# Performance work log

Measured on AMD Instinct MI355X. Metric: run time of the kernel, lower is better.

Reference implementation:

```python
import jax, jax.numpy as jnp
import numpy as np

B, S, D, H, E = 8, 2048, 1024, 4096, 8


def setup_inputs() -> dict:
    key = jax.random.key(0)
    k0, k1, k2, k3 = jax.random.split(key, 4)
    x = jax.random.normal(k0, (B, S, D), dtype=jnp.float32)
    # hash-router assignment: one expert per token, shape [B, S, 1] (top-k dim k=1)
    assign = jax.random.randint(k1, (B, S, 1), 0, E, dtype=jnp.int64)
    # per-expert Linear(dim, hidden): W_e [E, D, H], b_e [E, H]
    W_e = jax.random.normal(k2, (E, D, H), dtype=jnp.float32) * (1.0 / np.sqrt(D))
    b_e = jnp.zeros((E, H), dtype=jnp.float32)
    # shared output Linear(hidden, dim)
    W_out = jax.random.normal(k3, (H, D), dtype=jnp.float32) * (1.0 / np.sqrt(H))
    b_out = jnp.zeros((D,), dtype=jnp.float32)
    return {"x": x, "W_e": W_e, "b_e": b_e, "W_out": W_out, "b_out": b_out,
            "assign": assign}


def reference(x, W_e, b_e, W_out, b_out, assign):
    num_experts = W_e.shape[0]
    hidden = W_e.shape[2]
    # zero-init combine buffer, matching torch.zeros(batch, seq, hidden)
    expert_out = jnp.zeros(x.shape[:2] + (hidden,), dtype=x.dtype)
    for e in range(num_experts):  # fixed small expert loop
        y = jnp.einsum("bsd,dh->bsh", x, W_e[e]) + b_e[e]
        mask = (assign == e).any(-1)  # [B, S]
        expert_out = jnp.where(mask[..., None], y, expert_out)
    h = jax.nn.relu(expert_out)
    return jnp.einsum("bsh,hd->bsd", h, W_out) + b_out
```

## Files before the change

### kernel.cpp

```cpp
#include <hip/hip_runtime.h>
#include <hip/hip_bf16.h>
#include <stdint.h>

#define NB 8
#define NS 2048
#define ND 1024
#define NH 4096
#define NE 8
#define NTOK (NB*NS)

typedef __bf16 bf16;
typedef bf16 bf16x8 __attribute__((ext_vector_type(8)));
typedef float f32x4 __attribute__((ext_vector_type(4)));

static const size_t OFF_XB  = 128 * 1024;
static const size_t OFF_WTE = OFF_XB  + (size_t)NTOK * ND * 2;
static const size_t OFF_WTO = OFF_WTE + (size_t)NE * NH * ND * 2;
static const size_t OFF_HB  = OFF_WTO + (size_t)ND * NH * 2;
static const size_t WS_NEED = OFF_HB  + (size_t)NTOK * NH * 2;

#define GLDS16(src, dst) __builtin_amdgcn_global_load_lds( \
    (__attribute__((address_space(1))) void*)(void*)(src), \
    (__attribute__((address_space(3))) void*)(dst), 16, 0, 0)


__global__ void k_route(const int* __restrict__ assign, int* __restrict__ meta) {
    __shared__ int cnt[NE];
    __shared__ int offs_s[NE];
    int tid = threadIdx.x;
    if (tid < NE) cnt[tid] = 0;
    __syncthreads();
    for (int t = tid; t < NTOK; t += 1024) atomicAdd(&cnt[assign[t] & 7], 1);
    __syncthreads();
    if (tid == 0) {
        int o = 0;
        for (int e = 0; e < NE; e++) {
            meta[e] = cnt[e]; meta[16 + e] = o; offs_s[e] = o; o += cnt[e];
        }
    }
    __syncthreads();
    if (tid < NE) cnt[tid] = offs_s[tid];
    __syncthreads();
    int* perm = meta + 512;
    for (int t = tid; t < NTOK; t += 1024) {
        int e = assign[t] & 7;
        int p = atomicAdd(&cnt[e], 1);
        perm[p] = t;
    }
}

__global__ void k_gather_cvt(const float* __restrict__ x, const int* __restrict__ meta,
                             bf16* __restrict__ xbp) {
    long i = (long)blockIdx.x * blockDim.x + threadIdx.x;
    int row = (int)(i >> 7);
    int c8  = (int)(i & 127);
    const int* perm = meta + 512;
    int tok = perm[row];
    const float4* s = (const float4*)(x + (size_t)tok * ND + c8 * 8);
    float4 v0 = s[0], v1 = s[1];
    bf16x8 o;
    o[0] = (bf16)v0.x; o[1] = (bf16)v0.y; o[2] = (bf16)v0.z; o[3] = (bf16)v0.w;
    o[4] = (bf16)v1.x; o[5] = (bf16)v1.y; o[6] = (bf16)v1.z; o[7] = (bf16)v1.w;
    *(bf16x8*)(xbp + i * 8) = o;
}

__global__ void k_transpose(const float* __restrict__ in, bf16* __restrict__ out,
                            int R, int C) {
    __shared__ float tile[32][33];
    int b  = blockIdx.z;
    int c0 = blockIdx.x * 32, r0 = blockIdx.y * 32;
    const float* inb = in + (size_t)b * R * C;
    bf16* outb = out + (size_t)b * R * C;
    int tx = threadIdx.x, ty = threadIdx.y;
#pragma unroll
    for (int i = 0; i < 4; i++) {
        int r = r0 + ty + i * 8;
        tile[ty + i * 8][tx] = inb[(size_t)r * C + c0 + tx];
    }
    __syncthreads();
#pragma unroll
    for (int i = 0; i < 4; i++) {
        int c = c0 + ty + i * 8;
        outb[(size_t)c * R + r0 + tx] = (bf16)tile[tx][ty + i * 8];
    }
}


#define BAR { __builtin_amdgcn_s_barrier(); asm volatile("" ::: "memory"); }
#define VMC8 asm volatile("s_waitcnt vmcnt(8)" ::: "memory")
#define VMC0 asm volatile("s_waitcnt vmcnt(0)" ::: "memory")

#define LDA(msub) { \
  const char* Ab = sm + abuf + wr * 16384; \
  _Pragma("unroll") for (int m = 0; m < 4; m++) { \
    int row = ((msub) * 4 + m) * 16 + lr; \
    af[m][0] = *(const bf16x8*)(Ab + row * 128 + xk0); \
    af[m][1] = *(const bf16x8*)(Ab + row * 128 + xk1); \
  } }

#define LDB(nsub) { \
  const char* Bb = sm + bbuf + (wc >> 1) * 16384; \
  _Pragma("unroll") for (int n = 0; n < 2; n++) { \
    int row = (wc & 1) * 64 + ((nsub) * 2 + n) * 16 + lr; \
    bfr[(nsub)*2+n][0] = *(const bf16x8*)(Bb + row * 128 + xk0); \
    bfr[(nsub)*2+n][1] = *(const bf16x8*)(Bb + row * 128 + xk1); \
  } }

#define MFMA_Q(msub, nsub) { \
  __builtin_amdgcn_s_setprio(1); \
  _Pragma("unroll") for (int m = 0; m < 4; m++) \
  _Pragma("unroll") for (int n = 0; n < 2; n++) \
  _Pragma("unroll") for (int k = 0; k < 2; k++) \
    acc[(msub)*4+m][(nsub)*2+n] = __builtin_amdgcn_mfma_f32_16x16x32_bf16( \
        af[m][k], bfr[(nsub)*2+n][k], acc[(msub)*4+m][(nsub)*2+n], 0, 0, 0); \
  __builtin_amdgcn_s_setprio(0); }

#define DO_TILE(i, S0, S1, S2, S3, VW) { \
  const int abuf = ((i) % 3) * 32768; \
  const int bbuf = 98304 + ((i) & 1) * 32768; \
  LDA(0); LDB(0); S0; BAR; MFMA_Q(0,0); BAR; \
  LDB(1);         S1; BAR; MFMA_Q(0,1); BAR; \
  LDA(1);         S2; BAR; MFMA_Q(1,0); BAR; \
                  S3; VW; BAR; MFMA_Q(1,1); BAR; \
}

#define STAGE_A(t, h) { \
    char* d = sm + ((t) % 3) * 32768 + (h) * 16384 + wid * 1024; \
    GLDS16(srcA(t, h, 0), d); \
    GLDS16(srcA(t, h, 1), d + 8192); }
#define STAGE_B(t, h) { \
    char* d = sm + 98304 + ((t) & 1) * 32768 + (h) * 16384 + wid * 1024; \
    GLDS16(srcB(t, h, 0), d); \
    GLDS16(srcB(t, h, 1), d + 8192); }

__launch_bounds__(512, 2)
__global__ void k_gemm1(const bf16* __restrict__ xbp, const bf16* __restrict__ wte,
                        const float* __restrict__ b_e, bf16* __restrict__ hb,
                        const int* __restrict__ meta) {
    __shared__ __align__(16) char sm[163840];
    int f = blockIdx.x;
    int e = f & 7, q = f >> 3;
    int j = q % 9, bx = q / 9;
    int cnt = meta[e];
    int rs  = meta[16 + e] + j * 256;
    int rc  = cnt - j * 256; if (rc > 256) rc = 256;
    if (rc <= 0) return;
    int n0 = bx * 256;

    int tid = threadIdx.x;
    int lane = tid & 63, wid = tid >> 6;
    int wr = wid >> 2, wc = wid & 3;
    int lr = lane & 15, kg = lane >> 4;
    int xk0 = (kg ^ (lr & 7)) * 16;
    int xk1 = ((4 + kg) ^ (lr & 7)) * 16;

    int sr = tid >> 3, sl = tid & 7;
    int g = sl ^ (sr & 7);
    const bf16* pa[2][2];
#pragma unroll
    for (int h = 0; h < 2; h++)
#pragma unroll
      for (int rr = 0; rr < 2; rr++) {
        int arow = h * 128 + rr * 64 + sr;
        int p = rs + (arow < rc - 1 ? arow : rc - 1);
        pa[h][rr] = xbp + (size_t)p * ND + g * 8;
      }
    const bf16* pb0 = wte + ((size_t)e * NH + n0 + sr) * ND + g * 8;

#define srcA(t, h, rr) (pa[h][rr] + (size_t)(t) * 64)
#define srcB(t, h, rr) (pb0 + ((h) * 128 + (rr) * 64) * (size_t)ND + (size_t)(t) * 64)

    f32x4 acc[8][4] = {};
    bf16x8 af[4][2], bfr[4][2];
    const int NT = ND / 64;

    STAGE_A(0, 0); STAGE_A(0, 1); STAGE_B(0, 0); STAGE_B(0, 1);
    STAGE_A(1, 0); STAGE_A(1, 1); STAGE_B(1, 0); STAGE_B(1, 1);
    VMC8;
    BAR;

#pragma unroll 6
    for (int i = 0; i < NT - 2; i++)
        DO_TILE(i, STAGE_A(i + 2, 0), STAGE_A(i + 2, 1),
                   STAGE_B(i + 2, 0), STAGE_B(i + 2, 1), VMC8);
    DO_TILE(NT - 2, , , , , VMC0);
    DO_TILE(NT - 1, , , , , );

    float bias[4];
#pragma unroll
    for (int n = 0; n < 4; n++) bias[n] = b_e[e * NH + n0 + wc * 64 + n * 16 + lr];
#pragma unroll
    for (int m = 0; m < 8; m++) {
#pragma unroll
        for (int rr = 0; rr < 4; rr++) {
            int row = wr * 128 + m * 16 + kg * 4 + rr;
            if (row < rc) {
                bf16* hp = hb + (size_t)(rs + row) * NH + n0 + wc * 64;
#pragma unroll
                for (int n = 0; n < 4; n++)
                    hp[n * 16 + lr] = (bf16)fmaxf(acc[m][n][rr] + bias[n], 0.0f);
            }
        }
    }
#undef srcA
#undef srcB
}

__launch_bounds__(512, 2)
__global__ void k_gemm2(const bf16* __restrict__ hb, const bf16* __restrict__ wto,
                        const float* __restrict__ b_out, const int* __restrict__ meta,
                        float* __restrict__ out) {
    __shared__ __align__(16) char sm[163840];
    int lin = blockIdx.x;
    int swz = (lin & 7) * 32 + (lin >> 3);
    int bx = swz & 3, by = swz >> 2;
    int m0 = by * 256, n0 = bx * 256;
    const int* perm = meta + 512;

    int tid = threadIdx.x;
    int lane = tid & 63, wid = tid >> 6;
    int wr = wid >> 2, wc = wid & 3;
    int lr = lane & 15, kg = lane >> 4;
    int xk0 = (kg ^ (lr & 7)) * 16;
    int xk1 = ((4 + kg) ^ (lr & 7)) * 16;

    int sr = tid >> 3, sl = tid & 7;
    int g = sl ^ (sr & 7);
    const bf16* pa0 = hb  + ((size_t)m0 + sr) * NH + g * 8;
    const bf16* pb0 = wto + ((size_t)n0 + sr) * NH + g * 8;

#define srcA(t, h, rr) (pa0 + ((h) * 128 + (rr) * 64) * (size_t)NH + (size_t)(t) * 64)
#define srcB(t, h, rr) (pb0 + ((h) * 128 + (rr) * 64) * (size_t)NH + (size_t)(t) * 64)

    f32x4 acc[8][4] = {};
    bf16x8 af[4][2], bfr[4][2];
    const int NT = NH / 64;

    STAGE_A(0, 0); STAGE_A(0, 1); STAGE_B(0, 0); STAGE_B(0, 1);
    STAGE_A(1, 0); STAGE_A(1, 1); STAGE_B(1, 0); STAGE_B(1, 1);
    VMC8;
    BAR;

#pragma unroll 6
    for (int i = 0; i < NT - 2; i++)
        DO_TILE(i, STAGE_A(i + 2, 0), STAGE_A(i + 2, 1),
                   STAGE_B(i + 2, 0), STAGE_B(i + 2, 1), VMC8);
    DO_TILE(NT - 2, , , , , VMC0);
    DO_TILE(NT - 1, , , , , );

    float bias[4];
#pragma unroll
    for (int n = 0; n < 4; n++) bias[n] = b_out[n0 + wc * 64 + n * 16 + lr];
#pragma unroll
    for (int m = 0; m < 8; m++) {
#pragma unroll
        for (int rr = 0; rr < 4; rr++) {
            int prow = m0 + wr * 128 + m * 16 + kg * 4 + rr;
            int tok = perm[prow];
            float* op = out + (size_t)tok * ND + n0 + wc * 64;
#pragma unroll
            for (int n = 0; n < 4; n++)
                op[n * 16 + lr] = acc[m][n][rr] + bias[n];
        }
    }
#undef srcA
#undef srcB
}

extern "C" void kernel_launch(void* const* d_in, const int* in_sizes, int n_in,
                              void* d_out, int out_size, void* d_ws, size_t ws_size,
                              hipStream_t stream) {
    const float* x     = (const float*)d_in[0];
    const float* W_e   = (const float*)d_in[1];
    const float* b_e   = (const float*)d_in[2];
    const float* W_out = (const float*)d_in[3];
    const float* b_out = (const float*)d_in[4];
    const int*   assign = (const int*)d_in[5];
    float* out = (float*)d_out;

    if (ws_size < WS_NEED) return;

    char* ws = (char*)d_ws;
    int*  meta = (int*)ws;
    bf16* xbp = (bf16*)(ws + OFF_XB);
    bf16* wte = (bf16*)(ws + OFF_WTE);
    bf16* wto = (bf16*)(ws + OFF_WTO);
    bf16* hb  = (bf16*)(ws + OFF_HB);

    k_route<<<1, 1024, 0, stream>>>(assign, meta);
    k_gather_cvt<<<NTOK * ND / (256 * 8), 256, 0, stream>>>(x, meta, xbp);
    k_transpose<<<dim3(NH / 32, ND / 32, NE), dim3(32, 8), 0, stream>>>(W_e, wte, ND, NH);
    k_transpose<<<dim3(ND / 32, NH / 32, 1), dim3(32, 8), 0, stream>>>(W_out, wto, NH, ND);
    k_gemm1<<<1152, 512, 0, stream>>>(xbp, wte, b_e, hb, meta);
    k_gemm2<<<256, 512, 0, stream>>>(hb, wto, b_out, meta, out);
}
```

Before: 438.0 us.

## Fuse both expert GEMMs into one persistent cooperative kernel with grid sync

Merges the two GEMM kernels into a single cooperative kernel of 256 persistent blocks. Each block loops over up to five GEMM1 jobs, then a grid-wide sync precedes the GEMM2 tile. The intent is to remove a kernel launch and the inter-kernel gap. In exchange, GEMM1 work is distributed in fixed rounds, which can leave blocks idle where empty jobs cluster. The main-loop unroll is also reduced from 6 to 2, which may change instruction scheduling.

```diff
diff --git a/kernel.cpp b/kernel.cpp
--- a/kernel.cpp
+++ b/kernel.cpp
@@ -1,6 +1,9 @@
 #include <hip/hip_runtime.h>
+#include <hip/hip_cooperative_groups.h>
 #include <hip/hip_bf16.h>
 #include <stdint.h>
+
+namespace cg = cooperative_groups;
 
 #define NB 8
 #define NS 2048
@@ -134,137 +137,121 @@
     GLDS16(srcB(t, h, 1), d + 8192); }
 
 __launch_bounds__(512, 2)
-__global__ void k_gemm1(const bf16* __restrict__ xbp, const bf16* __restrict__ wte,
-                        const float* __restrict__ b_e, bf16* __restrict__ hb,
-                        const int* __restrict__ meta) {
+__global__ void k_moe(const bf16* __restrict__ xbp, const bf16* __restrict__ wte,
+                      const bf16* __restrict__ wto, const float* __restrict__ b_e,
+                      const float* __restrict__ b_out, bf16* __restrict__ hb,
+                      float* __restrict__ out, const int* __restrict__ meta) {
     __shared__ __align__(16) char sm[163840];
-    int f = blockIdx.x;
-    int e = f & 7, q = f >> 3;
-    int j = q % 9, bx = q / 9;
-    int cnt = meta[e];
-    int rs  = meta[16 + e] + j * 256;
-    int rc  = cnt - j * 256; if (rc > 256) rc = 256;
-    if (rc <= 0) return;
-    int n0 = bx * 256;
-
     int tid = threadIdx.x;
     int lane = tid & 63, wid = tid >> 6;
     int wr = wid >> 2, wc = wid & 3;
     int lr = lane & 15, kg = lane >> 4;
     int xk0 = (kg ^ (lr & 7)) * 16;
     int xk1 = ((4 + kg) ^ (lr & 7)) * 16;
-
     int sr = tid >> 3, sl = tid & 7;
     int g = sl ^ (sr & 7);
-    const bf16* pa[2][2];
-#pragma unroll
-    for (int h = 0; h < 2; h++)
-#pragma unroll
-      for (int rr = 0; rr < 2; rr++) {
-        int arow = h * 128 + rr * 64 + sr;
-        int p = rs + (arow < rc - 1 ? arow : rc - 1);
-        pa[h][rr] = xbp + (size_t)p * ND + g * 8;
-      }
-    const bf16* pb0 = wte + ((size_t)e * NH + n0 + sr) * ND + g * 8;
-
+    const int* perm = meta + 512;
+    int b = blockIdx.x;
+
+    for (int q = 0; q < 5; ++q) {
+        int job = q * 256 + b;
+        if (job >= 1152) break;
+        int e = job & 7, r2 = job >> 3;
+        int jj = r2 % 9, bx = r2 / 9;
+        int cnt = meta[e];
+        int rs = meta[16 + e] + jj * 256;
+        int rc = cnt - jj * 256; if (rc > 256) rc = 256;
+        if (rc > 0) {
+            int n0 = bx * 256;
+            const bf16* pa[2][2];
+#pragma unroll
+            for (int h = 0; h < 2; h++)
+#pragma unroll
+                for (int rr = 0; rr < 2; rr++) {
+                    int arow = h * 128 + rr * 64 + sr;
+                    int p = rs + (arow < rc - 1 ? arow : rc - 1);
+                    pa[h][rr] = xbp + (size_t)p * ND + g * 8;
+                }
+            const bf16* pb0 = wte + ((size_t)e * NH + n0 + sr) * ND + g * 8;
 #define srcA(t, h, rr) (pa[h][rr] + (size_t)(t) * 64)
 #define srcB(t, h, rr) (pb0 + ((h) * 128 + (rr) * 64) * (size_t)ND + (size_t)(t) * 64)
-
-    f32x4 acc[8][4] = {};
-    bf16x8 af[4][2], bfr[4][2];
-    const int NT = ND / 64;
-
-    STAGE_A(0, 0); STAGE_A(0, 1); STAGE_B(0, 0); STAGE_B(0, 1);
-    STAGE_A(1, 0); STAGE_A(1, 1); STAGE_B(1, 0); STAGE_B(1, 1);
-    VMC8;
-    BAR;
-
-#pragma unroll 6
-    for (int i = 0; i < NT - 2; i++)
-        DO_TILE(i, STAGE_A(i + 2, 0), STAGE_A(i + 2, 1),
-                   STAGE_B(i + 2, 0), STAGE_B(i + 2, 1), VMC8);
-    DO_TILE(NT - 2, , , , , VMC0);
-    DO_TILE(NT - 1, , , , , );
-
-    float bias[4];
-#pragma unroll
-    for (int n = 0; n < 4; n++) bias[n] = b_e[e * NH + n0 + wc * 64 + n * 16 + lr];
-#pragma unroll
-    for (int m = 0; m < 8; m++) {
-#pragma unroll
-        for (int rr = 0; rr < 4; rr++) {
-            int row = wr * 128 + m * 16 + kg * 4 + rr;
-            if (row < rc) {
-                bf16* hp = hb + (size_t)(rs + row) * NH + n0 + wc * 64;
-#pragma unroll
-                for (int n = 0; n < 4; n++)
-                    hp[n * 16 + lr] = (bf16)fmaxf(acc[m][n][rr] + bias[n], 0.0f);
+            f32x4 acc[8][4] = {};
+            bf16x8 af[4][2], bfr[4][2];
+            const int NT = ND / 64;
+            STAGE_A(0, 0); STAGE_A(0, 1); STAGE_B(0, 0); STAGE_B(0, 1);
+            STAGE_A(1, 0); STAGE_A(1, 1); STAGE_B(1, 0); STAGE_B(1, 1);
+            VMC8;
+            BAR;
+#pragma unroll 2
+            for (int i = 0; i < NT - 2; i++)
+                DO_TILE(i, STAGE_A(i + 2, 0), STAGE_A(i + 2, 1),
+                           STAGE_B(i + 2, 0), STAGE_B(i + 2, 1), VMC8);
+            DO_TILE(NT - 2, , , , , VMC0);
+            DO_TILE(NT - 1, , , , , );
+#undef srcA
+#undef srcB
+            float bias[4];
+#pragma unroll
+            for (int n = 0; n < 4; n++) bias[n] = b_e[e * NH + n0 + wc * 64 + n * 16 + lr];
+#pragma unroll
+            for (int m = 0; m < 8; m++) {
+#pragma unroll
+                for (int rr = 0; rr < 4; rr++) {
+                    int row = wr * 128 + m * 16 + kg * 4 + rr;
+                    if (row < rc) {
+                        bf16* hp = hb + (size_t)(rs + row) * NH + n0 + wc * 64;
+#pragma unroll
+                        for (int n = 0; n < 4; n++)
+                            hp[n * 16 + lr] = (bf16)fmaxf(acc[m][n][rr] + bias[n], 0.0f);
+                    }
+                }
             }
         }
-    }
+        __syncthreads();
+    }
+
+    __threadfence();
+    cg::this_grid().sync();
+
+    {
+        int swz = (b & 7) * 32 + (b >> 3);
+        int bx = swz & 3, by = swz >> 2;
+        int m0 = by * 256, n0 = bx * 256;
+        const bf16* pa0 = hb  + ((size_t)m0 + sr) * NH + g * 8;
+        const bf16* pb0 = wto + ((size_t)n0 + sr) * NH + g * 8;
+#define srcA(t, h, rr) (pa0 + ((h) * 128 + (rr) * 64) * (size_t)NH + (size_t)(t) * 64)
+#define srcB(t, h, rr) (pb0 + ((h) * 128 + (rr) * 64) * (size_t)NH + (size_t)(t) * 64)
+        f32x4 acc[8][4] = {};
+        bf16x8 af[4][2], bfr[4][2];
+        const int NT = NH / 64;
+        STAGE_A(0, 0); STAGE_A(0, 1); STAGE_B(0, 0); STAGE_B(0, 1);
+        STAGE_A(1, 0); STAGE_A(1, 1); STAGE_B(1, 0); STAGE_B(1, 1);
+        VMC8;
+        BAR;
+#pragma unroll 2
+        for (int i = 0; i < NT - 2; i++)
+            DO_TILE(i, STAGE_A(i + 2, 0), STAGE_A(i + 2, 1),
+                       STAGE_B(i + 2, 0), STAGE_B(i + 2, 1), VMC8);
+        DO_TILE(NT - 2, , , , , VMC0);
+        DO_TILE(NT - 1, , , , , );
 #undef srcA
 #undef srcB
-}
-
-__launch_bounds__(512, 2)
-__global__ void k_gemm2(const bf16* __restrict__ hb, const bf16* __restrict__ wto,
-                        const float* __restrict__ b_out, const int* __restrict__ meta,
-                        float* __restrict__ out) {
-    __shared__ __align__(16) char sm[163840];
-    int lin = blockIdx.x;
-    int swz = (lin & 7) * 32 + (lin >> 3);
-    int bx = swz & 3, by = swz >> 2;
-    int m0 = by * 256, n0 = bx * 256;
-    const int* perm = meta + 512;
-
-    int tid = threadIdx.x;
-    int lane = tid & 63, wid = tid >> 6;
-    int wr = wid >> 2, wc = wid & 3;
-    int lr = lane & 15, kg = lane >> 4;
-    int xk0 = (kg ^ (lr & 7)) * 16;
-    int xk1 = ((4 + kg) ^ (lr & 7)) * 16;
-
-    int sr = tid >> 3, sl = tid & 7;
-    int g = sl ^ (sr & 7);
-    const bf16* pa0 = hb  + ((size_t)m0 + sr) * NH + g * 8;
-    const bf16* pb0 = wto + ((size_t)n0 + sr) * NH + g * 8;
-
-#define srcA(t, h, rr) (pa0 + ((h) * 128 + (rr) * 64) * (size_t)NH + (size_t)(t) * 64)
-#define srcB(t, h, rr) (pb0 + ((h) * 128 + (rr) * 64) * (size_t)NH + (size_t)(t) * 64)
-
-    f32x4 acc[8][4] = {};
-    bf16x8 af[4][2], bfr[4][2];
-    const int NT = NH / 64;
-
-    STAGE_A(0, 0); STAGE_A(0, 1); STAGE_B(0, 0); STAGE_B(0, 1);
-    STAGE_A(1, 0); STAGE_A(1, 1); STAGE_B(1, 0); STAGE_B(1, 1);
-    VMC8;
-    BAR;
-
-#pragma unroll 6
-    for (int i = 0; i < NT - 2; i++)
-        DO_TILE(i, STAGE_A(i + 2, 0), STAGE_A(i + 2, 1),
-                   STAGE_B(i + 2, 0), STAGE_B(i + 2, 1), VMC8);
-    DO_TILE(NT - 2, , , , , VMC0);
-    DO_TILE(NT - 1, , , , , );
-
-    float bias[4];
-#pragma unroll
-    for (int n = 0; n < 4; n++) bias[n] = b_out[n0 + wc * 64 + n * 16 + lr];
-#pragma unroll
-    for (int m = 0; m < 8; m++) {
-#pragma unroll
-        for (int rr = 0; rr < 4; rr++) {
-            int prow = m0 + wr * 128 + m * 16 + kg * 4 + rr;
-            int tok = perm[prow];
-            float* op = out + (size_t)tok * ND + n0 + wc * 64;
-#pragma unroll
-            for (int n = 0; n < 4; n++)
-                op[n * 16 + lr] = acc[m][n][rr] + bias[n];
+        float bias[4];
+#pragma unroll
+        for (int n = 0; n < 4; n++) bias[n] = b_out[n0 + wc * 64 + n * 16 + lr];
+#pragma unroll
+        for (int m = 0; m < 8; m++) {
+#pragma unroll
+            for (int rr = 0; rr < 4; rr++) {
+                int prow = m0 + wr * 128 + m * 16 + kg * 4 + rr;
+                int tok = perm[prow];
+                float* op = out + (size_t)tok * ND + n0 + wc * 64;
+#pragma unroll
+                for (int n = 0; n < 4; n++)
+                    op[n * 16 + lr] = acc[m][n][rr] + bias[n];
+            }
         }
     }
-#undef srcA
-#undef srcB
 }
 
 extern "C" void kernel_launch(void* const* d_in, const int* in_sizes, int n_in,
@@ -282,15 +269,21 @@
 
     char* ws = (char*)d_ws;
     int*  meta = (int*)ws;
-    bf16* xbp = (bf16*)(ws + OFF_XB);
+    const bf16* xbp = (const bf16*)(ws + OFF_XB);
     bf16* wte = (bf16*)(ws + OFF_WTE);
     bf16* wto = (bf16*)(ws + OFF_WTO);
     bf16* hb  = (bf16*)(ws + OFF_HB);
 
     k_route<<<1, 1024, 0, stream>>>(assign, meta);
-    k_gather_cvt<<<NTOK * ND / (256 * 8), 256, 0, stream>>>(x, meta, xbp);
+    k_gather_cvt<<<NTOK * ND / (256 * 8), 256, 0, stream>>>(x, meta, (bf16*)(ws + OFF_XB));
     k_transpose<<<dim3(NH / 32, ND / 32, NE), dim3(32, 8), 0, stream>>>(W_e, wte, ND, NH);
     k_transpose<<<dim3(ND / 32, NH / 32, 1), dim3(32, 8), 0, stream>>>(W_out, wto, NH, ND);
-    k_gemm1<<<1152, 512, 0, stream>>>(xbp, wte, b_e, hb, meta);
-    k_gemm2<<<256, 512, 0, stream>>>(hb, wto, b_out, meta, out);
-}
+
+    const bf16* wte_c = wte;
+    const bf16* wto_c = wto;
+    const int*  meta_c = meta;
+    void* args[] = { (void*)&xbp, (void*)&wte_c, (void*)&wto_c, (void*)&b_e,
+                     (void*)&b_out, (void*)&hb, (void*)&out, (void*)&meta_c };
+    hipLaunchCooperativeKernel(reinterpret_cast<void*>(&k_moe),
+                               dim3(256), dim3(512), args, 0, stream);
+}
```

After: 452.7 us. 1.03x slower.

## Fuse token gather and bf16 conversion into gemm1 A-loading; merge weight transposes

Applied to the files above, without the earlier changes.

Removes the separate gather/convert kernel: gemm1 now loads fp32 rows of x through the routing permutation into registers, converts them to bf16 and writes them into swizzled shared memory, with double-buffered A and B. The two weight transpose launches are merged into a single kernel. This drops the intermediate bf16 x buffer round trip and one launch. In exchange, gemm1's A path moves from async global-to-LDS loads to register loads plus explicit LDS writes and lgkmcnt waits. The A pipeline also goes from triple to double buffering, which could expose more latency in gemm1.

```diff
diff --git a/kernel.cpp b/kernel.cpp
--- a/kernel.cpp
+++ b/kernel.cpp
@@ -49,62 +49,41 @@
     }
 }
 
-__global__ void k_gather_cvt(const float* __restrict__ x, const int* __restrict__ meta,
-                             bf16* __restrict__ xbp) {
-    long i = (long)blockIdx.x * blockDim.x + threadIdx.x;
-    int row = (int)(i >> 7);
-    int c8  = (int)(i & 127);
-    const int* perm = meta + 512;
-    int tok = perm[row];
-    const float4* s = (const float4*)(x + (size_t)tok * ND + c8 * 8);
-    float4 v0 = s[0], v1 = s[1];
-    bf16x8 o;
-    o[0] = (bf16)v0.x; o[1] = (bf16)v0.y; o[2] = (bf16)v0.z; o[3] = (bf16)v0.w;
-    o[4] = (bf16)v1.x; o[5] = (bf16)v1.y; o[6] = (bf16)v1.z; o[7] = (bf16)v1.w;
-    *(bf16x8*)(xbp + i * 8) = o;
-}
-
-__global__ void k_transpose(const float* __restrict__ in, bf16* __restrict__ out,
-                            int R, int C) {
+__global__ void k_transpose_all(const float* __restrict__ W_e, const float* __restrict__ W_out,
+                                bf16* __restrict__ wte, bf16* __restrict__ wto) {
     __shared__ float tile[32][33];
-    int b  = blockIdx.z;
-    int c0 = blockIdx.x * 32, r0 = blockIdx.y * 32;
-    const float* inb = in + (size_t)b * R * C;
-    bf16* outb = out + (size_t)b * R * C;
-    int tx = threadIdx.x, ty = threadIdx.y;
+    int b = blockIdx.x;
+    const float* in; bf16* outp; int R, C, c0, r0;
+    if (b < 8 * 128 * 32) {
+        int z = b >> 12, idx = b & 4095;
+        int bx = idx & 127, by = idx >> 7;
+        in = W_e + (size_t)z * ND * NH; outp = wte + (size_t)z * NH * ND;
+        R = ND; C = NH; c0 = bx * 32; r0 = by * 32;
+    } else {
+        int idx = b - 32768;
+        int bx = idx & 31, by = idx >> 5;
+        in = W_out; outp = wto;
+        R = NH; C = ND; c0 = bx * 32; r0 = by * 32;
+    }
+    int tx = threadIdx.x & 31, ty = threadIdx.x >> 5;
 #pragma unroll
     for (int i = 0; i < 4; i++) {
         int r = r0 + ty + i * 8;
-        tile[ty + i * 8][tx] = inb[(size_t)r * C + c0 + tx];
+        tile[ty + i * 8][tx] = in[(size_t)r * C + c0 + tx];
     }
     __syncthreads();
 #pragma unroll
     for (int i = 0; i < 4; i++) {
         int c = c0 + ty + i * 8;
-        outb[(size_t)c * R + r0 + tx] = (bf16)tile[tx][ty + i * 8];
+        outp[(size_t)c * R + r0 + tx] = (bf16)tile[tx][ty + i * 8];
     }
 }
 
 
 #define BAR { __builtin_amdgcn_s_barrier(); asm volatile("" ::: "memory"); }
+#define LGKM0 asm volatile("s_waitcnt lgkmcnt(0)" ::: "memory")
 #define VMC8 asm volatile("s_waitcnt vmcnt(8)" ::: "memory")
 #define VMC0 asm volatile("s_waitcnt vmcnt(0)" ::: "memory")
-
-#define LDA(msub) { \
-  const char* Ab = sm + abuf + wr * 16384; \
-  _Pragma("unroll") for (int m = 0; m < 4; m++) { \
-    int row = ((msub) * 4 + m) * 16 + lr; \
-    af[m][0] = *(const bf16x8*)(Ab + row * 128 + xk0); \
-    af[m][1] = *(const bf16x8*)(Ab + row * 128 + xk1); \
-  } }
-
-#define LDB(nsub) { \
-  const char* Bb = sm + bbuf + (wc >> 1) * 16384; \
-  _Pragma("unroll") for (int n = 0; n < 2; n++) { \
-    int row = (wc & 1) * 64 + ((nsub) * 2 + n) * 16 + lr; \
-    bfr[(nsub)*2+n][0] = *(const bf16x8*)(Bb + row * 128 + xk0); \
-    bfr[(nsub)*2+n][1] = *(const bf16x8*)(Bb + row * 128 + xk1); \
-  } }
 
 #define MFMA_Q(msub, nsub) { \
   __builtin_amdgcn_s_setprio(1); \
@@ -115,37 +94,58 @@
         af[m][k], bfr[(nsub)*2+n][k], acc[(msub)*4+m][(nsub)*2+n], 0, 0, 0); \
   __builtin_amdgcn_s_setprio(0); }
 
-#define DO_TILE(i, S0, S1, S2, S3, VW) { \
-  const int abuf = ((i) % 3) * 32768; \
-  const int bbuf = 98304 + ((i) & 1) * 32768; \
-  LDA(0); LDB(0); S0; BAR; MFMA_Q(0,0); BAR; \
-  LDB(1);         S1; BAR; MFMA_Q(0,1); BAR; \
-  LDA(1);         S2; BAR; MFMA_Q(1,0); BAR; \
-                  S3; VW; BAR; MFMA_Q(1,1); BAR; \
-}
-
-#define STAGE_A(t, h) { \
-    char* d = sm + ((t) % 3) * 32768 + (h) * 16384 + wid * 1024; \
-    GLDS16(srcA(t, h, 0), d); \
-    GLDS16(srcA(t, h, 1), d + 8192); }
-#define STAGE_B(t, h) { \
-    char* d = sm + 98304 + ((t) & 1) * 32768 + (h) * 16384 + wid * 1024; \
-    GLDS16(srcB(t, h, 0), d); \
-    GLDS16(srcB(t, h, 1), d + 8192); }
+
+#define G1_LDA(msub) { \
+  const char* Ab = sm + ((i) & 1) * 32768 + wr * 16384; \
+  _Pragma("unroll") for (int m = 0; m < 4; m++) { \
+    int row = ((msub) * 4 + m) * 16 + lr; \
+    af[m][0] = *(const bf16x8*)(Ab + row * 128 + xk0); \
+    af[m][1] = *(const bf16x8*)(Ab + row * 128 + xk1); \
+  } }
+
+#define G1_LDB(nsub) { \
+  const char* Bb = sm + 65536 + ((i) & 1) * 32768 + (wc >> 1) * 16384; \
+  _Pragma("unroll") for (int n = 0; n < 2; n++) { \
+    int row = (wc & 1) * 64 + ((nsub) * 2 + n) * 16 + lr; \
+    bfr[(nsub)*2+n][0] = *(const bf16x8*)(Bb + row * 128 + xk0); \
+    bfr[(nsub)*2+n][1] = *(const bf16x8*)(Bb + row * 128 + xk1); \
+  } }
+
+#define G1_ALOAD(t) { \
+  _Pragma("unroll") for (int h2 = 0; h2 < 2; h2++) \
+  _Pragma("unroll") for (int r2 = 0; r2 < 2; r2++) { \
+    const float4* s4 = (const float4*)(pax[h2][r2] + (size_t)(t) * 64); \
+    av[h2][r2][0] = s4[0]; av[h2][r2][1] = s4[1]; } }
+
+#define G1_AWRITE(t) { \
+  char* base = sm + ((t) & 1) * 32768; \
+  _Pragma("unroll") for (int h2 = 0; h2 < 2; h2++) \
+  _Pragma("unroll") for (int r2 = 0; r2 < 2; r2++) { \
+    float4 v0 = av[h2][r2][0], v1 = av[h2][r2][1]; \
+    bf16x8 o; \
+    o[0] = (bf16)v0.x; o[1] = (bf16)v0.y; o[2] = (bf16)v0.z; o[3] = (bf16)v0.w; \
+    o[4] = (bf16)v1.x; o[5] = (bf16)v1.y; o[6] = (bf16)v1.z; o[7] = (bf16)v1.w; \
+    *(bf16x8*)(base + h2 * 16384 + (r2 * 64 + sr) * 128 + wslot) = o; } }
+
+#define G1_STAGE_B(t, h) { \
+    char* d = sm + 65536 + ((t) & 1) * 32768 + (h) * 16384 + wid * 1024; \
+    GLDS16(pb0 + ((h) * 128) * (size_t)ND + (size_t)(t) * 64, d); \
+    GLDS16(pb0 + ((h) * 128 + 64) * (size_t)ND + (size_t)(t) * 64, d + 8192); }
 
 __launch_bounds__(512, 2)
-__global__ void k_gemm1(const bf16* __restrict__ xbp, const bf16* __restrict__ wte,
+__global__ void k_gemm1(const float* __restrict__ x, const bf16* __restrict__ wte,
                         const float* __restrict__ b_e, bf16* __restrict__ hb,
                         const int* __restrict__ meta) {
-    __shared__ __align__(16) char sm[163840];
+    __shared__ __align__(16) char sm[131072];
     int f = blockIdx.x;
     int e = f & 7, q = f >> 3;
-    int j = q % 9, bx = q / 9;
+    int jj = q % 9, bx = q / 9;
     int cnt = meta[e];
-    int rs  = meta[16 + e] + j * 256;
-    int rc  = cnt - j * 256; if (rc > 256) rc = 256;
+    int rs  = meta[16 + e] + jj * 256;
+    int rc  = cnt - jj * 256; if (rc > 256) rc = 256;
     if (rc <= 0) return;
     int n0 = bx * 256;
+    const int* perm = meta + 512;
 
     int tid = threadIdx.x;
     int lane = tid & 63, wid = tid >> 6;
@@ -155,36 +155,46 @@
     int xk1 = ((4 + kg) ^ (lr & 7)) * 16;
 
     int sr = tid >> 3, sl = tid & 7;
+    int wslot = (sl ^ (sr & 7)) * 16;
+    const float* pax[2][2];
+#pragma unroll
+    for (int h = 0; h < 2; h++)
+#pragma unroll
+        for (int rr = 0; rr < 2; rr++) {
+            int arow = h * 128 + rr * 64 + sr;
+            int p = rs + (arow < rc - 1 ? arow : rc - 1);
+            pax[h][rr] = x + (size_t)perm[p] * ND + sl * 8;
+        }
     int g = sl ^ (sr & 7);
-    const bf16* pa[2][2];
-#pragma unroll
-    for (int h = 0; h < 2; h++)
-#pragma unroll
-      for (int rr = 0; rr < 2; rr++) {
-        int arow = h * 128 + rr * 64 + sr;
-        int p = rs + (arow < rc - 1 ? arow : rc - 1);
-        pa[h][rr] = xbp + (size_t)p * ND + g * 8;
-      }
     const bf16* pb0 = wte + ((size_t)e * NH + n0 + sr) * ND + g * 8;
-
-#define srcA(t, h, rr) (pa[h][rr] + (size_t)(t) * 64)
-#define srcB(t, h, rr) (pb0 + ((h) * 128 + (rr) * 64) * (size_t)ND + (size_t)(t) * 64)
 
     f32x4 acc[8][4] = {};
     bf16x8 af[4][2], bfr[4][2];
+    float4 av[2][2][2];
     const int NT = ND / 64;
 
-    STAGE_A(0, 0); STAGE_A(0, 1); STAGE_B(0, 0); STAGE_B(0, 1);
-    STAGE_A(1, 0); STAGE_A(1, 1); STAGE_B(1, 0); STAGE_B(1, 1);
-    VMC8;
+    G1_ALOAD(0);
+    G1_STAGE_B(0, 0); G1_STAGE_B(0, 1);
+    G1_STAGE_B(1, 0); G1_STAGE_B(1, 1);
+    G1_AWRITE(0);
+    G1_ALOAD(1);
+    G1_AWRITE(1);
+    LGKM0;
+    VMC0;
     BAR;
 
-#pragma unroll 6
-    for (int i = 0; i < NT - 2; i++)
-        DO_TILE(i, STAGE_A(i + 2, 0), STAGE_A(i + 2, 1),
-                   STAGE_B(i + 2, 0), STAGE_B(i + 2, 1), VMC8);
-    DO_TILE(NT - 2, , , , , VMC0);
-    DO_TILE(NT - 1, , , , , );
+#pragma unroll 2
+    for (int i = 0; i < NT; i++) {
+        G1_LDA(0); G1_LDB(0); if (i + 1 < NT) G1_ALOAD(i + 1);
+        BAR; MFMA_Q(0,0); BAR;
+        G1_LDB(1);
+        BAR; MFMA_Q(0,1); BAR;
+        G1_LDA(1); if (i + 2 < NT) { G1_STAGE_B(i + 2, 0); }
+        BAR; MFMA_Q(1,0); BAR;
+        if (i + 2 < NT) { G1_STAGE_B(i + 2, 1); }
+        if (i + 1 < NT) { G1_AWRITE(i + 1); LGKM0; }
+        BAR; MFMA_Q(1,1); BAR;
+    }
 
     float bias[4];
 #pragma unroll
@@ -202,9 +212,42 @@
             }
         }
     }
-#undef srcA
-#undef srcB
-}
+}
+
+
+#define LDA2(msub) { \
+  const char* Ab = sm + abuf + wr * 16384; \
+  _Pragma("unroll") for (int m = 0; m < 4; m++) { \
+    int row = ((msub) * 4 + m) * 16 + lr; \
+    af[m][0] = *(const bf16x8*)(Ab + row * 128 + xk0); \
+    af[m][1] = *(const bf16x8*)(Ab + row * 128 + xk1); \
+  } }
+
+#define LDB2(nsub) { \
+  const char* Bb = sm + bbuf + (wc >> 1) * 16384; \
+  _Pragma("unroll") for (int n = 0; n < 2; n++) { \
+    int row = (wc & 1) * 64 + ((nsub) * 2 + n) * 16 + lr; \
+    bfr[(nsub)*2+n][0] = *(const bf16x8*)(Bb + row * 128 + xk0); \
+    bfr[(nsub)*2+n][1] = *(const bf16x8*)(Bb + row * 128 + xk1); \
+  } }
+
+#define DO_TILE2(i, S0, S1, S2, S3, VW) { \
+  const int abuf = ((i) % 3) * 32768; \
+  const int bbuf = 98304 + ((i) & 1) * 32768; \
+  LDA2(0); LDB2(0); S0; BAR; MFMA_Q(0,0); BAR; \
+  LDB2(1);          S1; BAR; MFMA_Q(0,1); BAR; \
+  LDA2(1);          S2; BAR; MFMA_Q(1,0); BAR; \
+                    S3; VW; BAR; MFMA_Q(1,1); BAR; \
+}
+
+#define STAGE_A2(t, h) { \
+    char* d = sm + ((t) % 3) * 32768 + (h) * 16384 + wid * 1024; \
+    GLDS16(pa0 + ((h) * 128) * (size_t)NH + (size_t)(t) * 64, d); \
+    GLDS16(pa0 + ((h) * 128 + 64) * (size_t)NH + (size_t)(t) * 64, d + 8192); }
+#define STAGE_B2(t, h) { \
+    char* d = sm + 98304 + ((t) & 1) * 32768 + (h) * 16384 + wid * 1024; \
+    GLDS16(pb0 + ((h) * 128) * (size_t)NH + (size_t)(t) * 64, d); \
+    GLDS16(pb0 + ((h) * 128 + 64) * (size_t)NH + (size_t)(t) * 64, d + 8192); }
 
 __launch_bounds__(512, 2)
 __global__ void k_gemm2(const bf16* __restrict__ hb, const bf16* __restrict__ wto,
@@ -229,24 +272,21 @@
     const bf16* pa0 = hb  + ((size_t)m0 + sr) * NH + g * 8;
     const bf16* pb0 = wto + ((size_t)n0 + sr) * NH + g * 8;
 
-#define srcA(t, h, rr) (pa0 + ((h) * 128 + (rr) * 64) * (size_t)NH + (size_t)(t) * 64)
-#define srcB(t, h, rr) (pb0 + ((h) * 128 + (rr) * 64) * (size_t)NH + (size_t)(t) * 64)
-
     f32x4 acc[8][4] = {};
     bf16x8 af[4][2], bfr[4][2];
     const int NT = NH / 64;
 
-    STAGE_A(0, 0); STAGE_A(0, 1); STAGE_B(0, 0); STAGE_B(0, 1);
-    STAGE_A(1, 0); STAGE_A(1, 1); STAGE_B(1, 0); STAGE_B(1, 1);
+    STAGE_A2(0, 0); STAGE_A2(0, 1); STAGE_B2(0, 0); STAGE_B2(0, 1);
+    STAGE_A2(1, 0); STAGE_A2(1, 1); STAGE_B2(1, 0); STAGE_B2(1, 1);
     VMC8;
     BAR;
 
 #pragma unroll 6
     for (int i = 0; i < NT - 2; i++)
-        DO_TILE(i, STAGE_A(i + 2, 0), STAGE_A(i + 2, 1),
-                   STAGE_B(i + 2, 0), STAGE_B(i + 2, 1), VMC8);
-    DO_TILE(NT - 2, , , , , VMC0);
-    DO_TILE(NT - 1, , , , , );
+        DO_TILE2(i, STAGE_A2(i + 2, 0), STAGE_A2(i + 2, 1),
+                    STAGE_B2(i + 2, 0), STAGE_B2(i + 2, 1), VMC8);
+    DO_TILE2(NT - 2, , , , , VMC0);
+    DO_TILE2(NT - 1, , , , , );
 
     float bias[4];
 #pragma unroll
@@ -263,8 +303,6 @@
                 op[n * 16 + lr] = acc[m][n][rr] + bias[n];
         }
     }
-#undef srcA
-#undef srcB
 }
 
 extern "C" void kernel_launch(void* const* d_in, const int* in_sizes, int n_in,
@@ -282,15 +320,12 @@
 
     char* ws = (char*)d_ws;
     int*  meta = (int*)ws;
-    bf16* xbp = (bf16*)(ws + OFF_XB);
     bf16* wte = (bf16*)(ws + OFF_WTE);
     bf16* wto = (bf16*)(ws + OFF_WTO);
     bf16* hb  = (bf16*)(ws + OFF_HB);
 
     k_route<<<1, 1024, 0, stream>>>(assign, meta);
-    k_gather_cvt<<<NTOK * ND / (256 * 8), 256, 0, stream>>>(x, meta, xbp);
-    k_transpose<<<dim3(NH / 32, ND / 32, NE), dim3(32, 8), 0, stream>>>(W_e, wte, ND, NH);
-    k_transpose<<<dim3(ND / 32, NH / 32, 1), dim3(32, 8), 0, stream>>>(W_out, wto, NH, ND);
-    k_gemm1<<<1152, 512, 0, stream>>>(xbp, wte, b_e, hb, meta);
+    k_transpose_all<<<36864, 256, 0, stream>>>(W_e, W_out, wte, wto);
+    k_gemm1<<<1152, 512, 0, stream>>>(x, wte, b_e, hb, meta);
     k_gemm2<<<256, 512, 0, stream>>>(hb, wto, b_out, meta, out);
 }
```

New measurement: 527.0 us. 20.3% more time.

## Restructure GEMM mainloop to 1024-thread blocks with simpler K-step pipeline

Applied to the files above, without the earlier changes.

Both GEMM kernels move from 512 threads with 8x4 accumulator tiles per wave to 1024 threads (16 waves) with 4x4 tiles per wave. The old four-quarter interleaved DO_TILE schedule is replaced by a two-half KSTEP: A is double-buffered and B triple-buffered, with the next A and the B two steps ahead issued between MFMA groups and sched_barriers fencing each group. The two weight transposes are merged into one launch. The aim is more waves to hide latency and lower register pressure per thread. The cost is more LDS fragment reads per MFMA, and launch_bounds(1024,4) cannot be met with 160KB of LDS per block.

```diff
diff --git a/kernel.cpp b/kernel.cpp
--- a/kernel.cpp
+++ b/kernel.cpp
@@ -64,207 +64,186 @@
     *(bf16x8*)(xbp + i * 8) = o;
 }
 
-__global__ void k_transpose(const float* __restrict__ in, bf16* __restrict__ out,
-                            int R, int C) {
+__global__ void k_transpose_all(const float* __restrict__ W_e, const float* __restrict__ W_out,
+                                bf16* __restrict__ wte, bf16* __restrict__ wto) {
     __shared__ float tile[32][33];
-    int b  = blockIdx.z;
-    int c0 = blockIdx.x * 32, r0 = blockIdx.y * 32;
-    const float* inb = in + (size_t)b * R * C;
-    bf16* outb = out + (size_t)b * R * C;
-    int tx = threadIdx.x, ty = threadIdx.y;
+    int b = blockIdx.x;
+    const float* in; bf16* outp; int R, C, c0, r0;
+    if (b < 32768) {
+        int z = b >> 12, idx = b & 4095;
+        int bx = idx & 127, by = idx >> 7;
+        in = W_e + (size_t)z * ND * NH; outp = wte + (size_t)z * NH * ND;
+        R = ND; C = NH; c0 = bx * 32; r0 = by * 32;
+    } else {
+        int idx = b - 32768;
+        int bx = idx & 31, by = idx >> 5;
+        in = W_out; outp = wto;
+        R = NH; C = ND; c0 = bx * 32; r0 = by * 32;
+    }
+    int tx = threadIdx.x & 31, ty = threadIdx.x >> 5;
 #pragma unroll
     for (int i = 0; i < 4; i++) {
         int r = r0 + ty + i * 8;
-        tile[ty + i * 8][tx] = inb[(size_t)r * C + c0 + tx];
+        tile[ty + i * 8][tx] = in[(size_t)r * C + c0 + tx];
     }
     __syncthreads();
 #pragma unroll
     for (int i = 0; i < 4; i++) {
         int c = c0 + ty + i * 8;
-        outb[(size_t)c * R + r0 + tx] = (bf16)tile[tx][ty + i * 8];
+        outp[(size_t)c * R + r0 + tx] = (bf16)tile[tx][ty + i * 8];
     }
 }
 
 
 #define BAR { __builtin_amdgcn_s_barrier(); asm volatile("" ::: "memory"); }
-#define VMC8 asm volatile("s_waitcnt vmcnt(8)" ::: "memory")
+#define VMC2 asm volatile("s_waitcnt vmcnt(2)" ::: "memory")
 #define VMC0 asm volatile("s_waitcnt vmcnt(0)" ::: "memory")
-
-#define LDA(msub) { \
-  const char* Ab = sm + abuf + wr * 16384; \
-  _Pragma("unroll") for (int m = 0; m < 4; m++) { \
-    int row = ((msub) * 4 + m) * 16 + lr; \
-    af[m][0] = *(const bf16x8*)(Ab + row * 128 + xk0); \
-    af[m][1] = *(const bf16x8*)(Ab + row * 128 + xk1); \
-  } }
-
-#define LDB(nsub) { \
-  const char* Bb = sm + bbuf + (wc >> 1) * 16384; \
-  _Pragma("unroll") for (int n = 0; n < 2; n++) { \
-    int row = (wc & 1) * 64 + ((nsub) * 2 + n) * 16 + lr; \
-    bfr[(nsub)*2+n][0] = *(const bf16x8*)(Bb + row * 128 + xk0); \
-    bfr[(nsub)*2+n][1] = *(const bf16x8*)(Bb + row * 128 + xk1); \
-  } }
-
-#define MFMA_Q(msub, nsub) { \
+#define SCB  __builtin_amdgcn_sched_barrier(0)
+
+#define FRAGS(xk) { \
+  _Pragma("unroll") for (int m = 0; m < 4; m++) \
+    af[m] = *(const bf16x8*)(Ab + (wm * 64 + m * 16 + lr) * 128 + (xk)); \
+  _Pragma("unroll") for (int n = 0; n < 4; n++) \
+    bf[n] = *(const bf16x8*)(Bb + (wn * 64 + n * 16 + lr) * 128 + (xk)); }
+
+#define MF16 { \
   __builtin_amdgcn_s_setprio(1); \
   _Pragma("unroll") for (int m = 0; m < 4; m++) \
-  _Pragma("unroll") for (int n = 0; n < 2; n++) \
-  _Pragma("unroll") for (int k = 0; k < 2; k++) \
-    acc[(msub)*4+m][(nsub)*2+n] = __builtin_amdgcn_mfma_f32_16x16x32_bf16( \
-        af[m][k], bfr[(nsub)*2+n][k], acc[(msub)*4+m][(nsub)*2+n], 0, 0, 0); \
+  _Pragma("unroll") for (int n = 0; n < 4; n++) \
+    acc[m][n] = __builtin_amdgcn_mfma_f32_16x16x32_bf16(af[m], bf[n], acc[m][n], 0, 0, 0); \
   __builtin_amdgcn_s_setprio(0); }
 
-#define DO_TILE(i, S0, S1, S2, S3, VW) { \
-  const int abuf = ((i) % 3) * 32768; \
-  const int bbuf = 98304 + ((i) & 1) * 32768; \
-  LDA(0); LDB(0); S0; BAR; MFMA_Q(0,0); BAR; \
-  LDB(1);         S1; BAR; MFMA_Q(0,1); BAR; \
-  LDA(1);         S2; BAR; MFMA_Q(1,0); BAR; \
-                  S3; VW; BAR; MFMA_Q(1,1); BAR; \
-}
-
-#define STAGE_A(t, h) { \
-    char* d = sm + ((t) % 3) * 32768 + (h) * 16384 + wid * 1024; \
-    GLDS16(srcA(t, h, 0), d); \
-    GLDS16(srcA(t, h, 1), d + 8192); }
-#define STAGE_B(t, h) { \
-    char* d = sm + 98304 + ((t) & 1) * 32768 + (h) * 16384 + wid * 1024; \
-    GLDS16(srcB(t, h, 0), d); \
-    GLDS16(srcB(t, h, 1), d + 8192); }
-
-__launch_bounds__(512, 2)
+#define STAGE_OP(baseoff, bufidx, p0, p1, koff) { \
+    char* d = sm + (baseoff) + (bufidx) * 32768 + tid * 16; \
+    GLDS16((p0) + (koff), d); \
+    GLDS16((p1) + (koff), d + 16384); }
+
+#define KSTEP(t, NT) { \
+  const char* Ab = sm + ((t) & 1) * 32768; \
+  const char* Bb = sm + 65536 + ((t) % 3) * 32768; \
+  bf16x8 af[4], bf[4]; \
+  FRAGS(xk0); \
+  if ((t) + 1 < (NT)) STAGE_OP(0, ((t) + 1) & 1, pa0, pa1, (size_t)((t) + 1) * 64); \
+  SCB; MF16; SCB; \
+  FRAGS(xk1); \
+  if ((t) + 2 < (NT)) STAGE_OP(65536, ((t) + 2) % 3, pb0, pb1, (size_t)((t) + 2) * 64); \
+  SCB; MF16; \
+  if ((t) + 2 < (NT)) { VMC2; } else { VMC0; } \
+  BAR; \
+}
+
+__launch_bounds__(1024, 4)
 __global__ void k_gemm1(const bf16* __restrict__ xbp, const bf16* __restrict__ wte,
                         const float* __restrict__ b_e, bf16* __restrict__ hb,
                         const int* __restrict__ meta) {
     __shared__ __align__(16) char sm[163840];
     int f = blockIdx.x;
     int e = f & 7, q = f >> 3;
-    int j = q % 9, bx = q / 9;
+    int jj = q % 9, bx = q / 9;
     int cnt = meta[e];
-    int rs  = meta[16 + e] + j * 256;
-    int rc  = cnt - j * 256; if (rc > 256) rc = 256;
+    int rs  = meta[16 + e] + jj * 256;
+    int rc  = cnt - jj * 256; if (rc > 256) rc = 256;
     if (rc <= 0) return;
     int n0 = bx * 256;
 
     int tid = threadIdx.x;
     int lane = tid & 63, wid = tid >> 6;
-    int wr = wid >> 2, wc = wid & 3;
+    int wm = wid >> 2, wn = wid & 3;
     int lr = lane & 15, kg = lane >> 4;
-    int xk0 = (kg ^ (lr & 7)) * 16;
+    int xk0 = ((kg)     ^ (lr & 7)) * 16;
     int xk1 = ((4 + kg) ^ (lr & 7)) * 16;
 
-    int sr = tid >> 3, sl = tid & 7;
-    int g = sl ^ (sr & 7);
-    const bf16* pa[2][2];
-#pragma unroll
-    for (int h = 0; h < 2; h++)
-#pragma unroll
-      for (int rr = 0; rr < 2; rr++) {
-        int arow = h * 128 + rr * 64 + sr;
-        int p = rs + (arow < rc - 1 ? arow : rc - 1);
-        pa[h][rr] = xbp + (size_t)p * ND + g * 8;
-      }
-    const bf16* pb0 = wte + ((size_t)e * NH + n0 + sr) * ND + g * 8;
-
-#define srcA(t, h, rr) (pa[h][rr] + (size_t)(t) * 64)
-#define srcB(t, h, rr) (pb0 + ((h) * 128 + (rr) * 64) * (size_t)ND + (size_t)(t) * 64)
-
-    f32x4 acc[8][4] = {};
-    bf16x8 af[4][2], bfr[4][2];
+    int srow = tid >> 3;
+    int g = (tid & 7) ^ (srow & 7);
+    int r0 = rs + (srow < rc - 1 ? srow : rc - 1);
+    int r1 = rs + (128 + srow < rc - 1 ? 128 + srow : rc - 1);
+    const bf16* pa0 = xbp + (size_t)r0 * ND + g * 8;
+    const bf16* pa1 = xbp + (size_t)r1 * ND + g * 8;
+    const bf16* pb0 = wte + ((size_t)e * NH + n0 + srow) * ND + g * 8;
+    const bf16* pb1 = pb0 + (size_t)128 * ND;
+
+    f32x4 acc[4][4] = {};
     const int NT = ND / 64;
 
-    STAGE_A(0, 0); STAGE_A(0, 1); STAGE_B(0, 0); STAGE_B(0, 1);
-    STAGE_A(1, 0); STAGE_A(1, 1); STAGE_B(1, 0); STAGE_B(1, 1);
-    VMC8;
+    STAGE_OP(0, 0, pa0, pa1, 0);
+    STAGE_OP(65536, 0, pb0, pb1, 0);
+    STAGE_OP(65536, 1, pb0, pb1, 64);
+    VMC2;
     BAR;
 
-#pragma unroll 6
-    for (int i = 0; i < NT - 2; i++)
-        DO_TILE(i, STAGE_A(i + 2, 0), STAGE_A(i + 2, 1),
-                   STAGE_B(i + 2, 0), STAGE_B(i + 2, 1), VMC8);
-    DO_TILE(NT - 2, , , , , VMC0);
-    DO_TILE(NT - 1, , , , , );
+#pragma unroll 2
+    for (int t = 0; t < NT; ++t) KSTEP(t, NT);
 
     float bias[4];
 #pragma unroll
-    for (int n = 0; n < 4; n++) bias[n] = b_e[e * NH + n0 + wc * 64 + n * 16 + lr];
-#pragma unroll
-    for (int m = 0; m < 8; m++) {
+    for (int n = 0; n < 4; n++) bias[n] = b_e[e * NH + n0 + wn * 64 + n * 16 + lr];
+#pragma unroll
+    for (int m = 0; m < 4; m++) {
 #pragma unroll
         for (int rr = 0; rr < 4; rr++) {
-            int row = wr * 128 + m * 16 + kg * 4 + rr;
+            int row = wm * 64 + m * 16 + kg * 4 + rr;
             if (row < rc) {
-                bf16* hp = hb + (size_t)(rs + row) * NH + n0 + wc * 64;
+                bf16* hp = hb + (size_t)(rs + row) * NH + n0 + wn * 64;
 #pragma unroll
                 for (int n = 0; n < 4; n++)
                     hp[n * 16 + lr] = (bf16)fmaxf(acc[m][n][rr] + bias[n], 0.0f);
             }
         }
     }
-#undef srcA
-#undef srcB
-}
-
-__launch_bounds__(512, 2)
+}
+
+__launch_bounds__(1024, 4)
 __global__ void k_gemm2(const bf16* __restrict__ hb, const bf16* __restrict__ wto,
                         const float* __restrict__ b_out, const int* __restrict__ meta,
                         float* __restrict__ out) {
     __shared__ __align__(16) char sm[163840];
     int lin = blockIdx.x;
     int swz = (lin & 7) * 32 + (lin >> 3);
-    int bx = swz & 3, by = swz >> 2;
-    int m0 = by * 256, n0 = bx * 256;
+    int bxn = swz & 3, by = swz >> 2;
+    int m0 = by * 256, n0 = bxn * 256;
     const int* perm = meta + 512;
 
     int tid = threadIdx.x;
     int lane = tid & 63, wid = tid >> 6;
-    int wr = wid >> 2, wc = wid & 3;
+    int wm = wid >> 2, wn = wid & 3;
     int lr = lane & 15, kg = lane >> 4;
-    int xk0 = (kg ^ (lr & 7)) * 16;
+    int xk0 = ((kg)     ^ (lr & 7)) * 16;
     int xk1 = ((4 + kg) ^ (lr & 7)) * 16;
 
-    int sr = tid >> 3, sl = tid & 7;
-    int g = sl ^ (sr & 7);
-    const bf16* pa0 = hb  + ((size_t)m0 + sr) * NH + g * 8;
-    const bf16* pb0 = wto + ((size_t)n0 + sr) * NH + g * 8;
-
-#define srcA(t, h, rr) (pa0 + ((h) * 128 + (rr) * 64) * (size_t)NH + (size_t)(t) * 64)
-#define srcB(t, h, rr) (pb0 + ((h) * 128 + (rr) * 64) * (size_t)NH + (size_t)(t) * 64)
-
-    f32x4 acc[8][4] = {};
-    bf16x8 af[4][2], bfr[4][2];
+    int srow = tid >> 3;
+    int g = (tid & 7) ^ (srow & 7);
+    const bf16* pa0 = hb  + ((size_t)m0 + srow) * NH + g * 8;
+    const bf16* pa1 = pa0 + (size_t)128 * NH;
+    const bf16* pb0 = wto + ((size_t)n0 + srow) * NH + g * 8;
+    const bf16* pb1 = pb0 + (size_t)128 * NH;
+
+    f32x4 acc[4][4] = {};
     const int NT = NH / 64;
 
-    STAGE_A(0, 0); STAGE_A(0, 1); STAGE_B(0, 0); STAGE_B(0, 1);
-    STAGE_A(1, 0); STAGE_A(1, 1); STAGE_B(1, 0); STAGE_B(1, 1);
-    VMC8;
+    STAGE_OP(0, 0, pa0, pa1, 0);
+    STAGE_OP(65536, 0, pb0, pb1, 0);
+    STAGE_OP(65536, 1, pb0, pb1, 64);
+    VMC2;
     BAR;
 
-#pragma unroll 6
-    for (int i = 0; i < NT - 2; i++)
-        DO_TILE(i, STAGE_A(i + 2, 0), STAGE_A(i + 2, 1),
-                   STAGE_B(i + 2, 0), STAGE_B(i + 2, 1), VMC8);
-    DO_TILE(NT - 2, , , , , VMC0);
-    DO_TILE(NT - 1, , , , , );
+#pragma unroll 2
+    for (int t = 0; t < NT; ++t) KSTEP(t, NT);
 
     float bias[4];
 #pragma unroll
-    for (int n = 0; n < 4; n++) bias[n] = b_out[n0 + wc * 64 + n * 16 + lr];
-#pragma unroll
-    for (int m = 0; m < 8; m++) {
+    for (int n = 0; n < 4; n++) bias[n] = b_out[n0 + wn * 64 + n * 16 + lr];
+#pragma unroll
+    for (int m = 0; m < 4; m++) {
 #pragma unroll
         for (int rr = 0; rr < 4; rr++) {
-            int prow = m0 + wr * 128 + m * 16 + kg * 4 + rr;
+            int prow = m0 + wm * 64 + m * 16 + kg * 4 + rr;
             int tok = perm[prow];
-            float* op = out + (size_t)tok * ND + n0 + wc * 64;
+            float* op = out + (size_t)tok * ND + n0 + wn * 64;
 #pragma unroll
             for (int n = 0; n < 4; n++)
                 op[n * 16 + lr] = acc[m][n][rr] + bias[n];
         }
     }
-#undef srcA
-#undef srcB
 }
 
 extern "C" void kernel_launch(void* const* d_in, const int* in_sizes, int n_in,
@@ -289,8 +268,7 @@
 
     k_route<<<1, 1024, 0, stream>>>(assign, meta);
     k_gather_cvt<<<NTOK * ND / (256 * 8), 256, 0, stream>>>(x, meta, xbp);
-    k_transpose<<<dim3(NH / 32, ND / 32, NE), dim3(32, 8), 0, stream>>>(W_e, wte, ND, NH);
-    k_transpose<<<dim3(ND / 32, NH / 32, 1), dim3(32, 8), 0, stream>>>(W_out, wto, NH, ND);
-    k_gemm1<<<1152, 512, 0, stream>>>(xbp, wte, b_e, hb, meta);
-    k_gemm2<<<256, 512, 0, stream>>>(hb, wto, b_out, meta, out);
-}
+    k_transpose_all<<<36864, 256, 0, stream>>>(W_e, W_out, wte, wto);
+    k_gemm1<<<1152, 1024, 0, stream>>>(xbp, wte, b_e, hb, meta);
+    k_gemm2<<<256, 1024, 0, stream>>>(hb, wto, b_out, meta, out);
+}
```

Result: slower. 512.9 us (+17.1%).
